# Performance work log

Hardware: AMD Instinct MI355X
Metric: run time of the kernel (lower is better)

Reference implementation:

```python
import jax, jax.numpy as jnp
import numpy as np
import math

H = 1024
B, S = 4, 2048

def setup_inputs() -> dict:
    key = jax.random.key(0)
    k0, k1, k2, k3, k4 = jax.random.split(key, 5)
    scale = 1.0 / math.sqrt(H)
    return {
        "input_seq_rep": jax.random.normal(k0, (B, S, H), dtype=jnp.float32),
        "Wk": jax.random.uniform(k1, (H, H), dtype=jnp.float32, minval=-scale, maxval=scale),
        "bk": jax.random.uniform(k2, (H,), dtype=jnp.float32, minval=-scale, maxval=scale),
        "Wq": jax.random.uniform(k3, (H, H), dtype=jnp.float32, minval=-scale, maxval=scale),
        "bq": jax.random.uniform(k4, (H,), dtype=jnp.float32, minval=-scale, maxval=scale),
        "k_mul": 64,
    }

def reference(input_seq_rep, Wk, bk, Wq, bq, k_mul):
    b, s, h = input_seq_rep.shape
    x = jax.nn.relu(input_seq_rep)
    # torch Linear: x @ W.T + b
    k = jnp.einsum('bsh,oh->bso', x, Wk) + bk   # key (also used as value)
    q = jnp.einsum('bsh,oh->bso', x, Wq) + bq
    scores = jnp.einsum('bqh,bkh->bqk', q, k) / jnp.sqrt(jnp.float32(h))
    # Faithful mask: banded window only for batch index 0; other batches all-zero mask
    i = jnp.arange(s)[:, None]
    j = jnp.arange(s)[None, :]
    band = ((j <= i) & (j >= i - k_mul)).astype(jnp.float32)  # (S,S)
    mask = jnp.zeros((b, s, s), dtype=jnp.float32).at[0].set(band)
    scores = jnp.where(mask == 0, jnp.float32(-1e9), scores)
    p_attn = jax.nn.softmax(scores, axis=-1)
    out = jnp.einsum('bqk,bkh->bqh', p_attn, k)
    return out, p_attn
```

## Files before the change

kernel.cpp:

```cpp
#include <hip/hip_runtime.h>

#define SD 2048
#define HD 1024
#define BD 4

typedef __bf16 bf16_t;
typedef bf16_t bf16x8 __attribute__((ext_vector_type(8)));
typedef float f32x4 __attribute__((ext_vector_type(4)));
typedef unsigned short ushortx8 __attribute__((ext_vector_type(8)));
typedef unsigned short ushort_t;

__device__ inline unsigned short f2bf(float f) {
  return __builtin_bit_cast(unsigned short, (__bf16)f);
}

__device__ inline float bf2f(unsigned short u) {
  return __builtin_bit_cast(float, (unsigned)u << 16);
}

__device__ inline void gload_lds16(const void* g, void* l) {
  __builtin_amdgcn_global_load_lds(
      (const __attribute__((address_space(1))) void*)g,
      (__attribute__((address_space(3))) void*)l, 16, 0, 0);
}

template <int ROWS>
__device__ inline void stage_rows(const ushort_t* __restrict__ src, int r0, int k0,
                                  int tid, ushort_t* lds)
{
#pragma unroll
  for (int it = 0; it < ROWS / 32; ++it) {
    int c   = it * 256 + tid;
    int row = c >> 3;
    int kc8 = c & 7;
    int kcs = kc8 ^ (row & 7);
    gload_lds16(&src[(size_t)(r0 + row) * HD + k0 + kcs * 8], &lds[c * 8]);
  }
}

__device__ inline bf16x8 lds_frag(const ushort_t* l, int row, int kc8) {
  int kcs = kc8 ^ (row & 7);
  return *(const bf16x8*)&l[row * 64 + kcs * 8];
}

__global__ __launch_bounds__(256) void prep(
    const float* __restrict__ X, const float* __restrict__ Wk,
    const float* __restrict__ Wq, ushort_t* __restrict__ Xb,
    ushort_t* __restrict__ Wkb, ushort_t* __restrict__ Wqb,
    float* __restrict__ part)
{
  const int bid = blockIdx.x;
  const int t = threadIdx.x;
  if (bid < 96) {
    const int b = bid >> 5;
    const int sub = bid & 31;
    const float4* Xp = (const float4*)(X + (size_t)(b + 1) * SD * HD + (size_t)sub * 64 * HD);
    float4 acc = make_float4(0.f, 0.f, 0.f, 0.f);
#pragma unroll 4
    for (int rr = 0; rr < 64; ++rr) {
      float4 v = Xp[rr * 256 + t];
      acc.x += fmaxf(v.x, 0.f); acc.y += fmaxf(v.y, 0.f);
      acc.z += fmaxf(v.z, 0.f); acc.w += fmaxf(v.w, 0.f);
    }
    ((float4*)part)[((size_t)b * 32 + sub) * 256 + t] = acc;
    return;
  }
  const int n8x = SD * HD / 8;
  const int n8w = HD * HD / 8;
  const int total = n8x + 2 * n8w;
  const int stride = 2048 * 256;
  for (int e = (bid - 96) * 256 + t; e < total; e += stride) {
    const float4* s4; ushortx8* d8; int idx; bool relu;
    if (e < n8x)            { s4 = (const float4*)X;  d8 = (ushortx8*)Xb;  idx = e;             relu = true; }
    else if (e < n8x + n8w) { s4 = (const float4*)Wk; d8 = (ushortx8*)Wkb; idx = e - n8x;       relu = false; }
    else                    { s4 = (const float4*)Wq; d8 = (ushortx8*)Wqb; idx = e - n8x - n8w; relu = false; }
    float4 a = s4[idx * 2], b4 = s4[idx * 2 + 1];
    float v[8] = {a.x, a.y, a.z, a.w, b4.x, b4.y, b4.z, b4.w};
    ushortx8 o;
#pragma unroll
    for (int j = 0; j < 8; ++j) {
      float f = v[j];
      if (relu) f = fmaxf(f, 0.0f);
      o[j] = f2bf(f);
    }
    d8[idx] = o;
  }
}

__global__ __launch_bounds__(256, 2) void gemm_kq(
    const ushort_t* __restrict__ Xb, const ushort_t* __restrict__ Wkb,
    const ushort_t* __restrict__ Wqb, const float* __restrict__ bk,
    const float* __restrict__ bq, ushort_t* __restrict__ Kb,
    ushort_t* __restrict__ Qb, float* __restrict__ patRest)
{
  __shared__ __align__(16) ushort_t lA[2][8192];
  __shared__ __align__(16) ushort_t lB[2][8192];

  const int bid = blockIdx.x;
  const int tid = threadIdx.x;

  if (bid >= 256) {
    const int f = bid - 256;
    const int nf4 = 3 * SD * (SD / 4);
    const float uf = 1.0f / SD;
    float4 v = make_float4(uf, uf, uf, uf);
    float4* p4 = (float4*)patRest;
    for (int e = f * 256 + tid; e < nf4; e += 384 * 256) p4[e] = v;
    return;
  }

  const int wg = ((bid & 7) << 5) | (bid >> 3);
  const int bm = wg >> 4, bn = wg & 15;
  const int half = bn >> 3;
  const ushort_t* Bm = half ? Wqb : Wkb;
  const int m0 = bm * 128, n0 = (bn & 7) * 128;

  const int lane = tid & 63;
  const int wave = tid >> 6;
  const int wm = wave >> 1, wn = wave & 1;

  f32x4 acc[4][4] = {};

  stage_rows<128>(Xb, m0, 0, tid, lA[0]);
  stage_rows<128>(Bm, n0, 0, tid, lB[0]);
  __syncthreads();

  for (int t = 0; t < 16; ++t) {
    const int cur = t & 1;
    if (t < 15) {
      stage_rows<128>(Xb, m0, (t + 1) * 64, tid, lA[cur ^ 1]);
      stage_rows<128>(Bm, n0, (t + 1) * 64, tid, lB[cur ^ 1]);
    }
#pragma unroll
    for (int h = 0; h < 2; ++h) {
      bf16x8 af[4], bfr[4];
#pragma unroll
      for (int mi = 0; mi < 4; ++mi)
        af[mi] = lds_frag(lA[cur], wm * 64 + mi * 16 + (lane & 15), h * 4 + (lane >> 4));
#pragma unroll
      for (int ni = 0; ni < 4; ++ni)
        bfr[ni] = lds_frag(lB[cur], wn * 64 + ni * 16 + (lane & 15), h * 4 + (lane >> 4));
#pragma unroll
      for (int mi = 0; mi < 4; ++mi)
#pragma unroll
        for (int ni = 0; ni < 4; ++ni)
          acc[mi][ni] = __builtin_amdgcn_mfma_f32_16x16x32_bf16(af[mi], bfr[ni], acc[mi][ni], 0, 0, 0);
    }
    __syncthreads();
  }

  const int rb = (lane >> 4) * 4;
  const int cc = lane & 15;
  const float* bias = half ? bq : bk;
  ushort_t* dst = half ? Qb : Kb;
#pragma unroll
  for (int ni = 0; ni < 4; ++ni) {
    int col = n0 + wn * 64 + ni * 16 + cc;
    float bv = bias[col];
#pragma unroll
    for (int mi = 0; mi < 4; ++mi) {
#pragma unroll
      for (int j = 0; j < 4; ++j) {
        int row = m0 + wm * 64 + mi * 16 + rb + j;
        dst[(size_t)row * HD + col] = f2bf(acc[mi][ni][j] + bv);
      }
    }
  }
}

__global__ __launch_bounds__(256, 2) void band_cm(
    const ushort_t* __restrict__ Q, const ushort_t* __restrict__ K,
    float* __restrict__ Sb0, float* __restrict__ Sb1,
    const float* __restrict__ part, const float* __restrict__ Wk,
    const float* __restrict__ bk, float* __restrict__ cm)
{
  __shared__ __align__(16) char smem[32768];
  const int bid = blockIdx.x;
  const int tid = threadIdx.x;

  if (bid < 126) {
    const int tt = bid >> 1;
    const int ks = bid & 1;
    const int blk = (tt + 1) >> 1;
    const int tcol = (tt + 1) & 1;
    const int m0 = blk * 64;
    const int n0 = (blk - 1 + tcol) * 64;
    float* Sb = ks ? Sb1 : Sb0;

    const int lane = tid & 63;
    const int wave = tid >> 6;
    const int wm = wave >> 1, wn = wave & 1;

    ushort_t* lA = (ushort_t*)smem;
    ushort_t* lB = (ushort_t*)(smem + 16384);

    f32x4 acc[2][2] = {};

    const int kbase = ks * 512;
    stage_rows<64>(Q, m0, kbase, tid, lA);
    stage_rows<64>(K, n0, kbase, tid, lB);
    __syncthreads();

    for (int t = 0; t < 8; ++t) {
      const int cur = t & 1;
      if (t < 7) {
        stage_rows<64>(Q, m0, kbase + (t + 1) * 64, tid, lA + (cur ^ 1) * 4096);
        stage_rows<64>(K, n0, kbase + (t + 1) * 64, tid, lB + (cur ^ 1) * 4096);
      }
#pragma unroll
      for (int h = 0; h < 2; ++h) {
        bf16x8 af[2], bfr[2];
#pragma unroll
        for (int mi = 0; mi < 2; ++mi)
          af[mi] = lds_frag(lA + cur * 4096, wm * 32 + mi * 16 + (lane & 15), h * 4 + (lane >> 4));
#pragma unroll
        for (int ni = 0; ni < 2; ++ni)
          bfr[ni] = lds_frag(lB + cur * 4096, wn * 32 + ni * 16 + (lane & 15), h * 4 + (lane >> 4));
#pragma unroll
        for (int mi = 0; mi < 2; ++mi)
#pragma unroll
          for (int ni = 0; ni < 2; ++ni)
            acc[mi][ni] = __builtin_amdgcn_mfma_f32_16x16x32_bf16(af[mi], bfr[ni], acc[mi][ni], 0, 0, 0);
      }
      __syncthreads();
    }

    const int rb = (lane >> 4) * 4;
    const int cc = lane & 15;
#pragma unroll
    for (int ni = 0; ni < 2; ++ni) {
      int ccol = tcol * 64 + wn * 32 + ni * 16 + cc;
#pragma unroll
      for (int mi = 0; mi < 2; ++mi)
#pragma unroll
        for (int j = 0; j < 4; ++j) {
          int row = m0 + wm * 32 + mi * 16 + rb + j;
          Sb[(size_t)row * 128 + ccol] = acc[mi][ni][j] * 0.03125f;
        }
    }
    return;
  }

  {
    const int cid = bid - 126;
    const int b = cid >> 4, og = cid & 15;
    float* xs = (float*)smem;
#pragma unroll
    for (int k = 0; k < 4; ++k) {
      int h = tid + 256 * k;
      float a = 0;
#pragma unroll 8
      for (int rc = 0; rc < 32; ++rc) a += part[((size_t)b * 32 + rc) * HD + h];
      xs[h] = a;
    }
    __syncthreads();
    const int o = og * 64 + (tid >> 2);
    const int q = tid & 3;
    const f32x4* wr = (const f32x4*)(Wk + (size_t)o * HD);
    const f32x4* x4 = (const f32x4*)xs;
    float a = 0;
#pragma unroll 8
    for (int i = 0; i < 64; ++i) {
      f32x4 w = wr[q * 64 + i], x = x4[q * 64 + i];
      a += w[0] * x[0] + w[1] * x[1] + w[2] * x[2] + w[3] * x[3];
    }
    a += __shfl_xor(a, 1);
    a += __shfl_xor(a, 2);
    if (q == 0) cm[b * HD + o] = a * (1.0f / SD) + bk[o];
  }
}

__global__ __launch_bounds__(256, 2) void pv_epi(
    const float* __restrict__ Sb0, const float* __restrict__ Sb1,
    const ushort_t* __restrict__ Kb, const float* __restrict__ cm,
    float* __restrict__ out0, float* __restrict__ P0,
    float* __restrict__ out123)
{
  __shared__ __align__(16) float smem[15488];
  const int bid = blockIdx.x;
  const int t = threadIdx.x;

  if (bid < 512) {
    float* Ks  = smem;
    float* spl = smem + 12288;
    const int i0 = (bid >> 3) * 32;
    const int hc = bid & 7;

    for (int e = t; e < 96 * 16; e += 256) {
      int lr = e >> 4, c8 = e & 15;
      int gr = i0 - 64 + lr;
      if (gr < 0) gr = 0;
      ushortx8 u = *(const ushortx8*)&Kb[(size_t)gr * HD + hc * 128 + c8 * 8];
      f32x4 f0 = {bf2f(u[0]), bf2f(u[1]), bf2f(u[2]), bf2f(u[3])};
      f32x4 f1 = {bf2f(u[4]), bf2f(u[5]), bf2f(u[6]), bf2f(u[7])};
      *(f32x4*)&Ks[lr * 128 + c8 * 8]     = f0;
      *(f32x4*)&Ks[lr * 128 + c8 * 8 + 4] = f1;
    }

    {
      const int r = t >> 3, sub = t & 7;
      const int i = i0 + r;
      const int jlo = (i >= 64) ? i - 64 : 0;
      const int scoff = i0 & 32;
      float sv[12];
      float m = -1e30f;
#pragma unroll
      for (int k = 0; k < 12; ++k) {
        int lj = sub + 8 * k;
        int gj = i0 - 64 + lj;
        bool val = (gj >= jlo) && (gj <= i);
        float s = -1e30f;
        if (val) {
          size_t sidx = (size_t)i * 128 + lj + scoff;
          s = Sb0[sidx] + Sb1[sidx];
        }
        sv[k] = s;
        m = fmaxf(m, s);
      }
#pragma unroll
      for (int off = 1; off < 8; off <<= 1) m = fmaxf(m, __shfl_xor(m, off));
      float p[12], sum = 0;
#pragma unroll
      for (int k = 0; k < 12; ++k) {
        p[k] = (sv[k] > -1e29f) ? __expf(sv[k] - m) : 0.0f;
        sum += p[k];
      }
#pragma unroll
      for (int off = 1; off < 8; off <<= 1) sum += __shfl_xor(sum, off);
      float inv = 1.0f / sum;
#pragma unroll
      for (int k = 0; k < 12; ++k) spl[r * 100 + sub + 8 * k] = p[k] * inv;
    }
    __syncthreads();

    const int r = t >> 3;
    const int g = t & 7;
    f32x4 a0 = {0,0,0,0}, a1 = {0,0,0,0}, a2 = {0,0,0,0}, a3 = {0,0,0,0};
    for (int lj = 0; lj < 96; ++lj) {
      float pv = spl[r * 100 + lj];
      const float* kr = &Ks[lj * 128 + g * 4];
      a0 += pv * *(const f32x4*)(kr);
      a1 += pv * *(const f32x4*)(kr + 32);
      a2 += pv * *(const f32x4*)(kr + 64);
      a3 += pv * *(const f32x4*)(kr + 96);
    }
    float* ob = out0 + (size_t)(i0 + r) * HD + hc * 128 + g * 4;
    *(f32x4*)(ob)      = a0;
    *(f32x4*)(ob + 32) = a1;
    *(f32x4*)(ob + 64) = a2;
    *(f32x4*)(ob + 96) = a3;
    return;
  }

  if (bid < 1024) {
    float* probs = smem;
    const int widx = t >> 6;
    const int lane = t & 63;
    const int i = (bid - 512) * 4 + widx;
    const int jlo = (i >= 64) ? i - 64 : 0;
    const int cnt = i - jlo + 1;
    const int base = ((i >> 6) - 1) * 64;

    float s0 = -1e30f;
    if (lane < cnt) {
      size_t c = (size_t)i * 128 + (jlo - base + lane);
      s0 = Sb0[c] + Sb1[c];
    }
    float s1 = -1e30f;
    if (cnt == 65) {
      size_t c = (size_t)i * 128 + (jlo - base + 64);
      s1 = Sb0[c] + Sb1[c];
    }
    float m = s0;
#pragma unroll
    for (int off = 1; off < 64; off <<= 1) m = fmaxf(m, __shfl_xor(m, off));
    m = fmaxf(m, s1);
    float p0 = (lane < cnt) ? __expf(s0 - m) : 0.0f;
    float p1 = (cnt == 65) ? __expf(s1 - m) : 0.0f;
    float sum = p0;
#pragma unroll
    for (int off = 1; off < 64; off <<= 1) sum += __shfl_xor(sum, off);
    sum += p1;
    float inv = 1.0f / sum;
    if (lane < cnt) probs[widx * 68 + lane] = p0 * inv;
    if (lane == 0 && cnt == 65) probs[widx * 68 + 64] = p1 * inv;
    __syncthreads();

    float4* rowp = (float4*)(P0 + (size_t)i * SD);
#pragma unroll
    for (int k = 0; k < 8; ++k) {
      int f4i = k * 64 + lane;
      int j0 = f4i * 4;
      float4 v = make_float4(0.f, 0.f, 0.f, 0.f);
      if (j0 + 3 >= jlo && j0 <= i) {
        float* vv = (float*)&v;
#pragma unroll
        for (int q = 0; q < 4; ++q) {
          int j = j0 + q;
          if (j >= jlo && j <= i) vv[q] = probs[widx * 68 + (j - jlo)];
        }
      }
      rowp[f4i] = v;
    }
    return;
  }

  {
    const int nf4 = 3 * SD * (HD / 4);
    const int per_b = SD * (HD / 4);
    const f32x4* cm4 = (const f32x4*)cm;
    f32x4* o4 = (f32x4*)out123;
    for (int idx = (bid - 1024) * 256 + t; idx < nf4; idx += 512 * 256) {
      int b = idx / per_b;
      int h4 = idx & (HD / 4 - 1);
      o4[idx] = cm4[b * (HD / 4) + h4];
    }
  }
}

extern "C" void kernel_launch(void* const* d_in, const int* in_sizes, int n_in,
                              void* d_out, int out_size, void* d_ws, size_t ws_size,
                              hipStream_t stream)
{
  (void)in_sizes; (void)n_in; (void)out_size; (void)ws_size;
  const float* X  = (const float*)d_in[0];
  const float* Wk = (const float*)d_in[1];
  const float* bk = (const float*)d_in[2];
  const float* Wq = (const float*)d_in[3];
  const float* bq = (const float*)d_in[4];

  float* out = (float*)d_out;
  float* pat = out + (size_t)BD * SD * HD;

  char* w = (char*)d_ws;
  ushort_t* Xb   = (ushort_t*)w; w += (size_t)SD * HD * 2;
  ushort_t* Wkb  = (ushort_t*)w; w += (size_t)HD * HD * 2;
  ushort_t* Wqb  = (ushort_t*)w; w += (size_t)HD * HD * 2;
  ushort_t* Kb0  = (ushort_t*)w; w += (size_t)SD * HD * 2;
  ushort_t* Q0b  = (ushort_t*)w; w += (size_t)SD * HD * 2;
  float*    part = (float*)w;    w += (size_t)3 * 32 * HD * 4;
  float*    cm   = (float*)w;    w += (size_t)3 * HD * 4;
  float*    Sb0  = (float*)w;    w += (size_t)SD * 128 * 4;
  float*    Sb1  = (float*)w;    w += (size_t)SD * 128 * 4;

  prep<<<2144, 256, 0, stream>>>(X, Wk, Wq, Xb, Wkb, Wqb, part);
  gemm_kq<<<640, 256, 0, stream>>>(Xb, Wkb, Wqb, bk, bq, Kb0, Q0b, pat + (size_t)SD * SD);
  band_cm<<<174, 256, 0, stream>>>(Q0b, Kb0, Sb0, Sb1, part, Wk, bk, cm);
  pv_epi<<<1536, 256, 0, stream>>>(Sb0, Sb1, Kb0, cm, out, pat, out + (size_t)SD * HD);
}
```

Baseline: 73.47 us.

## Split-K the K/Q projection GEMM and add a reduce kernel with fill work

The K/Q projection GEMM now splits the reduction dimension in two, launching 512 tiles instead of 256, and writes fp32 partials to a new workspace buffer. A new reduce_fill kernel sums the two partials, adds bias, converts to bf16, and also takes over the cm computation and the uniform p_attn fill. The band-score GEMM becomes its own kernel. The aim is better CU occupancy for the GEMM, at the cost of about 32MB of extra fp32 partial writes and reads plus one more kernel launch.

```diff
diff --git a/kernel.cpp b/kernel.cpp
--- a/kernel.cpp
+++ b/kernel.cpp
@@ -89,31 +89,20 @@
 
 __global__ __launch_bounds__(256, 2) void gemm_kq(
     const ushort_t* __restrict__ Xb, const ushort_t* __restrict__ Wkb,
-    const ushort_t* __restrict__ Wqb, const float* __restrict__ bk,
-    const float* __restrict__ bq, ushort_t* __restrict__ Kb,
-    ushort_t* __restrict__ Qb, float* __restrict__ patRest)
+    const ushort_t* __restrict__ Wqb, float* __restrict__ Pp)
 {
   __shared__ __align__(16) ushort_t lA[2][8192];
   __shared__ __align__(16) ushort_t lB[2][8192];
 
   const int bid = blockIdx.x;
   const int tid = threadIdx.x;
-
-  if (bid >= 256) {
-    const int f = bid - 256;
-    const int nf4 = 3 * SD * (SD / 4);
-    const float uf = 1.0f / SD;
-    float4 v = make_float4(uf, uf, uf, uf);
-    float4* p4 = (float4*)patRest;
-    for (int e = f * 256 + tid; e < nf4; e += 384 * 256) p4[e] = v;
-    return;
-  }
-
-  const int wg = ((bid & 7) << 5) | (bid >> 3);
+  const int ks = bid >> 8;
+  const int tile = bid & 255;
+  const int wg = ((tile & 7) << 5) | (tile >> 3);
   const int bm = wg >> 4, bn = wg & 15;
-  const int half = bn >> 3;
-  const ushort_t* Bm = half ? Wqb : Wkb;
+  const ushort_t* Bm = (bn >= 8) ? Wqb : Wkb;
   const int m0 = bm * 128, n0 = (bn & 7) * 128;
+  const int kb = ks * 512;
 
   const int lane = tid & 63;
   const int wave = tid >> 6;
@@ -121,15 +110,15 @@
 
   f32x4 acc[4][4] = {};
 
-  stage_rows<128>(Xb, m0, 0, tid, lA[0]);
-  stage_rows<128>(Bm, n0, 0, tid, lB[0]);
+  stage_rows<128>(Xb, m0, kb, tid, lA[0]);
+  stage_rows<128>(Bm, n0, kb, tid, lB[0]);
   __syncthreads();
 
-  for (int t = 0; t < 16; ++t) {
+  for (int t = 0; t < 8; ++t) {
     const int cur = t & 1;
-    if (t < 15) {
-      stage_rows<128>(Xb, m0, (t + 1) * 64, tid, lA[cur ^ 1]);
-      stage_rows<128>(Bm, n0, (t + 1) * 64, tid, lB[cur ^ 1]);
+    if (t < 7) {
+      stage_rows<128>(Xb, m0, kb + (t + 1) * 64, tid, lA[cur ^ 1]);
+      stage_rows<128>(Bm, n0, kb + (t + 1) * 64, tid, lB[cur ^ 1]);
     }
 #pragma unroll
     for (int h = 0; h < 2; ++h) {
@@ -151,111 +140,71 @@
 
   const int rb = (lane >> 4) * 4;
   const int cc = lane & 15;
-  const float* bias = half ? bq : bk;
-  ushort_t* dst = half ? Qb : Kb;
+  float* P = Pp + (size_t)ks * SD * SD;
 #pragma unroll
   for (int ni = 0; ni < 4; ++ni) {
-    int col = n0 + wn * 64 + ni * 16 + cc;
-    float bv = bias[col];
+    int gcol = bn * 128 + wn * 64 + ni * 16 + cc;
 #pragma unroll
     for (int mi = 0; mi < 4; ++mi) {
 #pragma unroll
       for (int j = 0; j < 4; ++j) {
         int row = m0 + wm * 64 + mi * 16 + rb + j;
-        dst[(size_t)row * HD + col] = f2bf(acc[mi][ni][j] + bv);
+        P[(size_t)row * SD + gcol] = acc[mi][ni][j];
       }
     }
   }
 }
 
-__global__ __launch_bounds__(256, 2) void band_cm(
-    const ushort_t* __restrict__ Q, const ushort_t* __restrict__ K,
-    float* __restrict__ Sb0, float* __restrict__ Sb1,
-    const float* __restrict__ part, const float* __restrict__ Wk,
-    const float* __restrict__ bk, float* __restrict__ cm)
-{
-  __shared__ __align__(16) char smem[32768];
+__global__ __launch_bounds__(256) void reduce_fill(
+    const float* __restrict__ Pp, const float* __restrict__ bk,
+    const float* __restrict__ bq, ushort_t* __restrict__ Kb,
+    ushort_t* __restrict__ Qb, const float* __restrict__ part,
+    const float* __restrict__ Wk, float* __restrict__ cm,
+    float* __restrict__ patRest)
+{
+  __shared__ float xs[HD];
   const int bid = blockIdx.x;
-  const int tid = threadIdx.x;
-
-  if (bid < 126) {
-    const int tt = bid >> 1;
-    const int ks = bid & 1;
-    const int blk = (tt + 1) >> 1;
-    const int tcol = (tt + 1) & 1;
-    const int m0 = blk * 64;
-    const int n0 = (blk - 1 + tcol) * 64;
-    float* Sb = ks ? Sb1 : Sb0;
-
-    const int lane = tid & 63;
-    const int wave = tid >> 6;
-    const int wm = wave >> 1, wn = wave & 1;
-
-    ushort_t* lA = (ushort_t*)smem;
-    ushort_t* lB = (ushort_t*)(smem + 16384);
-
-    f32x4 acc[2][2] = {};
-
-    const int kbase = ks * 512;
-    stage_rows<64>(Q, m0, kbase, tid, lA);
-    stage_rows<64>(K, n0, kbase, tid, lB);
-    __syncthreads();
-
-    for (int t = 0; t < 8; ++t) {
-      const int cur = t & 1;
-      if (t < 7) {
-        stage_rows<64>(Q, m0, kbase + (t + 1) * 64, tid, lA + (cur ^ 1) * 4096);
-        stage_rows<64>(K, n0, kbase + (t + 1) * 64, tid, lB + (cur ^ 1) * 4096);
-      }
-#pragma unroll
-      for (int h = 0; h < 2; ++h) {
-        bf16x8 af[2], bfr[2];
-#pragma unroll
-        for (int mi = 0; mi < 2; ++mi)
-          af[mi] = lds_frag(lA + cur * 4096, wm * 32 + mi * 16 + (lane & 15), h * 4 + (lane >> 4));
-#pragma unroll
-        for (int ni = 0; ni < 2; ++ni)
-          bfr[ni] = lds_frag(lB + cur * 4096, wn * 32 + ni * 16 + (lane & 15), h * 4 + (lane >> 4));
-#pragma unroll
-        for (int mi = 0; mi < 2; ++mi)
-#pragma unroll
-          for (int ni = 0; ni < 2; ++ni)
-            acc[mi][ni] = __builtin_amdgcn_mfma_f32_16x16x32_bf16(af[mi], bfr[ni], acc[mi][ni], 0, 0, 0);
-      }
-      __syncthreads();
-    }
-
-    const int rb = (lane >> 4) * 4;
-    const int cc = lane & 15;
-#pragma unroll
-    for (int ni = 0; ni < 2; ++ni) {
-      int ccol = tcol * 64 + wn * 32 + ni * 16 + cc;
-#pragma unroll
-      for (int mi = 0; mi < 2; ++mi)
-#pragma unroll
-        for (int j = 0; j < 4; ++j) {
-          int row = m0 + wm * 32 + mi * 16 + rb + j;
-          Sb[(size_t)row * 128 + ccol] = acc[mi][ni][j] * 0.03125f;
-        }
+  const int t = threadIdx.x;
+
+  if (bid < 256) {
+    const float* P0 = Pp;
+    const float* P1 = Pp + (size_t)SD * SD;
+#pragma unroll
+    for (int it = 0; it < 8; ++it) {
+      int e8 = (bid * 256 + t) + it * 65536;
+      size_t base = (size_t)e8 * 8;
+      int row = e8 >> 8;
+      int col = (e8 & 255) * 8;
+      f32x4 a0 = *(const f32x4*)&P0[base], a1 = *(const f32x4*)&P0[base + 4];
+      f32x4 b0 = *(const f32x4*)&P1[base], b1 = *(const f32x4*)&P1[base + 4];
+      const float* bias = (col < 1024) ? bk : bq;
+      int bc = col & 1023;
+      f32x4 v0 = *(const f32x4*)&bias[bc], v1 = *(const f32x4*)&bias[bc + 4];
+      a0 += b0 + v0; a1 += b1 + v1;
+      ushortx8 o;
+#pragma unroll
+      for (int j = 0; j < 4; ++j) { o[j] = f2bf(a0[j]); o[4 + j] = f2bf(a1[j]); }
+      ushort_t* dst = (col < 1024) ? &Kb[(size_t)row * HD + bc]
+                                   : &Qb[(size_t)row * HD + bc];
+      *(ushortx8*)dst = o;
     }
     return;
   }
 
-  {
-    const int cid = bid - 126;
+  if (bid < 304) {
+    const int cid = bid - 256;
     const int b = cid >> 4, og = cid & 15;
-    float* xs = (float*)smem;
 #pragma unroll
     for (int k = 0; k < 4; ++k) {
-      int h = tid + 256 * k;
+      int h = t + 256 * k;
       float a = 0;
 #pragma unroll 8
       for (int rc = 0; rc < 32; ++rc) a += part[((size_t)b * 32 + rc) * HD + h];
       xs[h] = a;
     }
     __syncthreads();
-    const int o = og * 64 + (tid >> 2);
-    const int q = tid & 3;
+    const int o = og * 64 + (t >> 2);
+    const int q = t & 3;
     const f32x4* wr = (const f32x4*)(Wk + (size_t)o * HD);
     const f32x4* x4 = (const f32x4*)xs;
     float a = 0;
@@ -267,6 +216,85 @@
     a += __shfl_xor(a, 1);
     a += __shfl_xor(a, 2);
     if (q == 0) cm[b * HD + o] = a * (1.0f / SD) + bk[o];
+    return;
+  }
+
+  {
+    const int f = bid - 304;
+    const int nf4 = 3 * SD * (SD / 4);
+    const float uf = 1.0f / SD;
+    float4 v = make_float4(uf, uf, uf, uf);
+    float4* p4 = (float4*)patRest;
+    for (int e = f * 256 + t; e < nf4; e += 384 * 256) p4[e] = v;
+  }
+}
+
+__global__ __launch_bounds__(256, 2) void band(
+    const ushort_t* __restrict__ Q, const ushort_t* __restrict__ K,
+    float* __restrict__ Sb0, float* __restrict__ Sb1)
+{
+  __shared__ __align__(16) char smem[32768];
+  const int bid = blockIdx.x;
+  const int tid = threadIdx.x;
+
+  const int tt = bid >> 1;
+  const int ks = bid & 1;
+  const int blk = (tt + 1) >> 1;
+  const int tcol = (tt + 1) & 1;
+  const int m0 = blk * 64;
+  const int n0 = (blk - 1 + tcol) * 64;
+  float* Sb = ks ? Sb1 : Sb0;
+
+  const int lane = tid & 63;
+  const int wave = tid >> 6;
+  const int wm = wave >> 1, wn = wave & 1;
+
+  ushort_t* lA = (ushort_t*)smem;
+  ushort_t* lB = (ushort_t*)(smem + 16384);
+
+  f32x4 acc[2][2] = {};
+
+  const int kbase = ks * 512;
+  stage_rows<64>(Q, m0, kbase, tid, lA);
+  stage_rows<64>(K, n0, kbase, tid, lB);
+  __syncthreads();
+
+  for (int t = 0; t < 8; ++t) {
+    const int cur = t & 1;
+    if (t < 7) {
+      stage_rows<64>(Q, m0, kbase + (t + 1) * 64, tid, lA + (cur ^ 1) * 4096);
+      stage_rows<64>(K, n0, kbase + (t + 1) * 64, tid, lB + (cur ^ 1) * 4096);
+    }
+#pragma unroll
+    for (int h = 0; h < 2; ++h) {
+      bf16x8 af[2], bfr[2];
+#pragma unroll
+      for (int mi = 0; mi < 2; ++mi)
+        af[mi] = lds_frag(lA + cur * 4096, wm * 32 + mi * 16 + (lane & 15), h * 4 + (lane >> 4));
+#pragma unroll
+      for (int ni = 0; ni < 2; ++ni)
+        bfr[ni] = lds_frag(lB + cur * 4096, wn * 32 + ni * 16 + (lane & 15), h * 4 + (lane >> 4));
+#pragma unroll
+      for (int mi = 0; mi < 2; ++mi)
+#pragma unroll
+        for (int ni = 0; ni < 2; ++ni)
+          acc[mi][ni] = __builtin_amdgcn_mfma_f32_16x16x32_bf16(af[mi], bfr[ni], acc[mi][ni], 0, 0, 0);
+    }
+    __syncthreads();
+  }
+
+  const int rb = (lane >> 4) * 4;
+  const int cc = lane & 15;
+#pragma unroll
+  for (int ni = 0; ni < 2; ++ni) {
+    int ccol = tcol * 64 + wn * 32 + ni * 16 + cc;
+#pragma unroll
+    for (int mi = 0; mi < 2; ++mi)
+#pragma unroll
+      for (int j = 0; j < 4; ++j) {
+        int row = m0 + wm * 32 + mi * 16 + rb + j;
+        Sb[(size_t)row * 128 + ccol] = acc[mi][ni][j] * 0.03125f;
+      }
   }
 }
 
@@ -442,9 +470,12 @@
   float*    cm   = (float*)w;    w += (size_t)3 * HD * 4;
   float*    Sb0  = (float*)w;    w += (size_t)SD * 128 * 4;
   float*    Sb1  = (float*)w;    w += (size_t)SD * 128 * 4;
+  float*    Pp   = (float*)w;    w += (size_t)2 * SD * SD * 4;
 
   prep<<<2144, 256, 0, stream>>>(X, Wk, Wq, Xb, Wkb, Wqb, part);
-  gemm_kq<<<640, 256, 0, stream>>>(Xb, Wkb, Wqb, bk, bq, Kb0, Q0b, pat + (size_t)SD * SD);
-  band_cm<<<174, 256, 0, stream>>>(Q0b, Kb0, Sb0, Sb1, part, Wk, bk, cm);
+  gemm_kq<<<512, 256, 0, stream>>>(Xb, Wkb, Wqb, Pp);
+  reduce_fill<<<688, 256, 0, stream>>>(Pp, bk, bq, Kb0, Q0b, part, Wk, cm,
+                                       pat + (size_t)SD * SD);
+  band<<<126, 256, 0, stream>>>(Q0b, Kb0, Sb0, Sb1);
   pv_epi<<<1536, 256, 0, stream>>>(Sb0, Sb1, Kb0, cm, out, pat, out + (size_t)SD * HD);
 }
```

Result: slower. 81.15 us (+10.5%).
